# Kernel tuning notes

Measured on AMD Instinct MI355X. Metric: run time of the kernel, lower is better.

Reference implementation:

```python
import jax, jax.numpy as jnp
import numpy as np

N0, N1, N2, N3, B = 120000, 20000, 6000, 1600, 64
E1, E2, E3 = 480000, 144000, 38400
KS = 5  # kernel size per dim; K = 125 total


def spline_basis(pseudo, ks=KS):
    # open B-spline basis, degree 1, over [0,1]^3 (torch_spline_conv semantics)
    p = pseudo * (ks - 1)                       # (E,3)
    lo = jnp.clip(jnp.floor(p), 0.0, ks - 2.0)  # (E,3)
    f = p - lo                                  # fractional part
    bits = jnp.array([[(s >> d) & 1 for d in range(3)] for s in range(8)],
                     dtype=jnp.float32)         # (8,3) corner offsets
    w = jnp.where(bits[None] > 0, f[:, None, :], 1.0 - f[:, None, :])  # (E,8,3)
    basis = w[..., 0] * w[..., 1] * w[..., 2]   # (E,8)
    strides = jnp.array([1.0, ks, ks * ks], dtype=jnp.float32)
    kidx = ((lo[:, None, :] + bits[None]) * strides).sum(-1).astype(jnp.int32)  # (E,8)
    return basis, kidx


def spline_conv(x, edge_index, pseudo, W, root, bias, num_nodes):
    src, dst = edge_index[0], edge_index[1]
    basis, kidx = spline_basis(pseudo)                   # (E,8), (E,8)
    XW = jnp.einsum('ni,kio->nko', x, W)                 # (N,K,out)
    taps = XW[src[:, None], kidx]                        # (E,8,out) gather
    msg = (taps * basis[..., None]).sum(axis=1)          # (E,out)
    agg = jax.ops.segment_sum(msg, dst, num_segments=num_nodes)
    deg = jax.ops.segment_sum(jnp.ones_like(dst, jnp.float32), dst,
                              num_segments=num_nodes)
    agg = agg / jnp.maximum(deg, 1.0)[:, None]           # mean aggregation
    return agg + x @ root + bias


def seg_max(x, seg, n):
    v = jax.ops.segment_max(x, seg, num_segments=n)
    return jnp.where(jnp.isfinite(v), v, 0.0)  # empty voxels -> 0


def setup_inputs() -> dict:
    key = jax.random.key(0)
    ks = jax.random.split(key, 24)
    return {
        'x0': jax.random.uniform(ks[0], (N0, 1), jnp.float32),
        'cluster0': jax.random.randint(ks[1], (N0,), 0, N1),
        'edge1': jax.random.randint(ks[2], (2, E1), 0, N1),
        'pseudo1': jax.random.uniform(ks[3], (E1, 3), jnp.float32),
        'W1': jax.random.normal(ks[4], (125, 1, 64), jnp.float32) * 0.1,
        'root1': jax.random.normal(ks[5], (1, 64), jnp.float32) * 0.1,
        'b1': jnp.zeros((64,), jnp.float32),
        'cluster1': jax.random.randint(ks[6], (N1,), 0, N2),
        'edge2': jax.random.randint(ks[7], (2, E2), 0, N2),
        'pseudo2': jax.random.uniform(ks[8], (E2, 3), jnp.float32),
        'W2': jax.random.normal(ks[9], (125, 64, 64), jnp.float32) * 0.05,
        'root2': jax.random.normal(ks[10], (64, 64), jnp.float32) * 0.05,
        'b2': jnp.zeros((64,), jnp.float32),
        'cluster2': jax.random.randint(ks[11], (N2,), 0, N3),
        'edge3': jax.random.randint(ks[12], (2, E3), 0, N3),
        'pseudo3': jax.random.uniform(ks[13], (E3, 3), jnp.float32),
        'W3': jax.random.normal(ks[14], (125, 64, 128), jnp.float32) * 0.05,
        'root3': jax.random.normal(ks[15], (64, 128), jnp.float32) * 0.05,
        'b3': jnp.zeros((128,), jnp.float32),
        'cluster3': jax.random.randint(ks[16], (N3,), 0, B * 8),
        'fc1_w': jax.random.normal(ks[17], (1024, 256), jnp.float32) * 0.03,
        'fc1_b': jnp.zeros((256,), jnp.float32),
        'fc2_w': jax.random.normal(ks[18], (256, 10), jnp.float32) * 0.06,
        'fc2_b': jnp.zeros((10,), jnp.float32),
    }


def reference(x0, cluster0, edge1, pseudo1, W1, root1, b1,
              cluster1, edge2, pseudo2, W2, root2, b2,
              cluster2, edge3, pseudo3, W3, root3, b3,
              cluster3, fc1_w, fc1_b, fc2_w, fc2_b):
    x = seg_max(x0, cluster0, N1)                       # sparse voxel max pool 1
    x = jax.nn.elu(spline_conv(x, edge1, pseudo1, W1, root1, b1, N1))
    x = seg_max(x, cluster1, N2)                        # pool 2
    x = jax.nn.elu(spline_conv(x, edge2, pseudo2, W2, root2, b2, N2))
    x = seg_max(x, cluster2, N3)                        # pool 3
    x = jax.nn.elu(spline_conv(x, edge3, pseudo3, W3, root3, b3, N3))
    x = seg_max(x, cluster3, B * 8)                     # dense 2x2x2 voxel pool
    x = x.reshape(B, 8 * 128)
    x = jax.nn.elu(x @ fc1_w + fc1_b)
    x = x @ fc2_w + fc2_b
    return jax.nn.log_softmax(x, axis=1)
```

## Files before the change

### kernel.cpp

```cpp
#include <hip/hip_runtime.h>
#include <hip/hip_bf16.h>
#include <math.h>

#define N0c 120000
#define N1c 20000
#define N2c 6000
#define N3c 1600
#define E1c 480000
#define E2c 144000
#define E3c 38400

#define HB1 32
#define HB2 120
#define HB3 40
#define WT2B 125
#define WT3B 250
#define SS0B 469

typedef __attribute__((ext_vector_type(8))) short short8;
typedef __attribute__((ext_vector_type(4))) float f32x4;

__device__ __forceinline__ float eluf(float x) {
    return x > 0.0f ? x : expm1f(x);
}

__device__ __forceinline__ unsigned f2sort(float f) {
    unsigned u = __float_as_uint(f);
    return (u & 0x80000000u) ? ~u : (u | 0x80000000u);
}
__device__ __forceinline__ float sort2f(unsigned u) {
    unsigned bits = (u & 0x80000000u) ? (u & 0x7FFFFFFFu) : ~u;
    return __uint_as_float(bits);
}
__device__ __forceinline__ unsigned short f2bf(float v) {
    unsigned u = __float_as_uint(v);
    unsigned r = (u + 0x7FFFu + ((u >> 16) & 1u)) >> 16;
    return (unsigned short)r;
}

__global__ __launch_bounds__(256) void hist_all(
    const int* __restrict__ edge1, const int* __restrict__ edge2,
    const int* __restrict__ edge3,
    const float* __restrict__ pseudo2, const float* __restrict__ pseudo3,
    const float* __restrict__ W2, const float* __restrict__ W3,
    const float* __restrict__ x0, const int* __restrict__ cluster0,
    int* __restrict__ blockCnt1,
    int* __restrict__ blockCnt2, int* __restrict__ cntD2,
    int* __restrict__ blockCnt3, int* __restrict__ cntD3,
    unsigned short* __restrict__ W2t, unsigned short* __restrict__ W3t,
    unsigned* __restrict__ xm1)
{
    __shared__ float tile[64][65];
    int b = blockIdx.x, t = threadIdx.x;
    if (b < HB1) {
        int* h = (int*)tile;
        for (int i = t; i < 1250; i += 256) h[i] = 0;
        __syncthreads();
        for (int e = b * 256 + t; e < E1c; e += HB1 * 256)
            atomicAdd(&h[edge1[E1c + e] >> 4], 1);
        __syncthreads();
        for (int i = t; i < 1250; i += 256) blockCnt1[i * HB1 + b] = h[i];
    } else if (b < HB1 + HB2 + HB3) {
        int* h = (int*)tile;
        bool is2 = b < HB1 + HB2;
        int rb = is2 ? (b - HB1) : (b - HB1 - HB2);
        int nblk = is2 ? HB2 : HB3;
        int E = is2 ? E2c : E3c;
        const int* edge = is2 ? edge2 : edge3;
        const float* pseudo = is2 ? pseudo2 : pseudo3;
        int* blockCnt = is2 ? blockCnt2 : blockCnt3;
        int* dstCnt = is2 ? cntD2 : cntD3;
        if (t < 64) h[t] = 0;
        __syncthreads();
        for (int e = rb * 256 + t; e < E; e += nblk * 256) {
            int c = 0, mul = 1;
            #pragma unroll
            for (int d = 0; d < 3; d++) {
                float p = pseudo[e * 3 + d] * 4.0f;
                float l = fminf(fmaxf(floorf(p), 0.0f), 3.0f);
                c += (int)l * mul;
                mul <<= 2;
            }
            atomicAdd(&h[c], 1);
            atomicAdd(&dstCnt[edge[E + e]], 1);
        }
        __syncthreads();
        if (t < 64) blockCnt[t * nblk + rb] = h[t];
    } else if (b < HB1 + HB2 + HB3 + WT2B) {
        int k = b - (HB1 + HB2 + HB3);
        int col = t & 63, rq = t >> 6;
        #pragma unroll
        for (int i = 0; i < 16; i++) {
            int ic = i * 4 + rq;
            tile[ic][col] = W2[((size_t)k * 64 + ic) * 64 + col];
        }
        __syncthreads();
        int n = t >> 2, icq = (t & 3) * 16;
        unsigned* dst = (unsigned*)(W2t + ((size_t)k * 64 + n) * 64 + icq);
        #pragma unroll
        for (int j = 0; j < 8; j++) {
            unsigned lo = f2bf(tile[icq + 2 * j][n]);
            unsigned hi = f2bf(tile[icq + 2 * j + 1][n]);
            dst[j] = lo | (hi << 16);
        }
    } else if (b < HB1 + HB2 + HB3 + WT2B + WT3B) {
        int b2 = b - (HB1 + HB2 + HB3 + WT2B);
        int k = b2 >> 1, half = (b2 & 1) * 64;
        int col = t & 63, rq = t >> 6;
        #pragma unroll
        for (int i = 0; i < 16; i++) {
            int ic = i * 4 + rq;
            tile[ic][col] = W3[((size_t)k * 64 + ic) * 128 + half + col];
        }
        __syncthreads();
        int n = t >> 2, icq = (t & 3) * 16;
        unsigned* dst = (unsigned*)(W3t + ((size_t)k * 128 + half + n) * 64 + icq);
        #pragma unroll
        for (int j = 0; j < 8; j++) {
            unsigned lo = f2bf(tile[icq + 2 * j][n]);
            unsigned hi = f2bf(tile[icq + 2 * j + 1][n]);
            dst[j] = lo | (hi << 16);
        }
    } else {
        int idx = (b - (HB1 + HB2 + HB3 + WT2B + WT3B)) * 256 + t;
        if (idx < N0c)
            atomicMax(&xm1[cluster0[idx]], f2sort(x0[idx]));
    }
}

__global__ __launch_bounds__(256) void plan_all(
    const int* __restrict__ blockCnt1, int* __restrict__ start1,
    int* __restrict__ blockOff1,
    const int* __restrict__ blockCnt2, int* __restrict__ binCnt2,
    int* __restrict__ binStart2, int* __restrict__ blkPrefix2,
    int* __restrict__ chunkBin2, int* __restrict__ chunkOff2,
    int* __restrict__ blockOff2,
    const int* __restrict__ blockCnt3, int* __restrict__ binCnt3,
    int* __restrict__ binStart3, int* __restrict__ blkPrefix3,
    int* __restrict__ chunkBin3, int* __restrict__ chunkOff3,
    int* __restrict__ blockOff3)
{
    __shared__ int ps[256];
    __shared__ int ps64[64];
    int t = threadIdx.x;

    int loc[5];
    int s = 0;
    #pragma unroll
    for (int i = 0; i < 5; i++) {
        int bin = t * 5 + i;
        int v = 0;
        if (bin < 1250) {
            const int4* row = (const int4*)(blockCnt1 + (size_t)bin * HB1);
            #pragma unroll
            for (int j = 0; j < HB1 / 4; j++) {
                int4 q = row[j];
                v += q.x + q.y + q.z + q.w;
            }
        }
        loc[i] = v;
        s += v;
    }
    ps[t] = s;
    __syncthreads();
    for (int ofs = 1; ofs < 256; ofs <<= 1) {
        int add = (t >= ofs) ? ps[t - ofs] : 0;
        __syncthreads();
        ps[t] += add;
        __syncthreads();
    }
    int run = (t == 0) ? 0 : ps[t - 1];
    #pragma unroll
    for (int i = 0; i < 5; i++) {
        int bin = t * 5 + i;
        if (bin < 1250) {
            start1[bin] = run;
            run += loc[i];
        }
    }
    if (t == 255) start1[1250] = run;
    __syncthreads();

    if (t < 64) {
        int v = 0;
        const int4* row = (const int4*)(blockCnt2 + (size_t)t * HB2);
        for (int j = 0; j < HB2 / 4; j++) {
            int4 q = row[j];
            v += q.x + q.y + q.z + q.w;
        }
        binCnt2[t] = v;
        ps64[t] = v;
    }
    __syncthreads();
    if (t == 0) {
        int s2 = 0, p = 0;
        for (int c = 0; c < 64; c++) {
            int v = ps64[c];
            binStart2[c] = s2;
            blkPrefix2[c] = p;
            s2 += v;
            p += (v + 63) >> 6;
        }
        binStart2[64] = s2;
        blkPrefix2[64] = p;
    }
    __syncthreads();
    if (t < 64) {
        int nch = (binCnt2[t] + 63) >> 6;
        int base = blkPrefix2[t];
        for (int j = 0; j < nch; j++) {
            chunkBin2[base + j] = t;
            chunkOff2[base + j] = j;
        }
    }
    __syncthreads();

    if (t < 64) {
        int v = 0;
        const int4* row = (const int4*)(blockCnt3 + (size_t)t * HB3);
        for (int j = 0; j < HB3 / 4; j++) {
            int4 q = row[j];
            v += q.x + q.y + q.z + q.w;
        }
        binCnt3[t] = v;
        ps64[t] = v;
    }
    __syncthreads();
    if (t == 0) {
        int s3 = 0, p = 0;
        for (int c = 0; c < 64; c++) {
            int v = ps64[c];
            binStart3[c] = s3;
            blkPrefix3[c] = p;
            s3 += v;
            p += (v + 63) >> 6;
        }
        binStart3[64] = s3;
        blkPrefix3[64] = p;
    }
    __syncthreads();
    if (t < 64) {
        int nch = (binCnt3[t] + 63) >> 6;
        int base = blkPrefix3[t];
        for (int j = 0; j < nch; j++) {
            chunkBin3[base + j] = t;
            chunkOff3[base + j] = j;
        }
    }
    __syncthreads();

    for (int r = t; r < 1250; r += 256) {
        int rn = start1[r];
        const int* c = blockCnt1 + (size_t)r * HB1;
        int* o = blockOff1 + (size_t)r * HB1;
        #pragma unroll 4
        for (int bb = 0; bb < HB1; bb++) { o[bb] = rn; rn += c[bb]; }
    }
    if (t < 64) {
        int rn = binStart2[t];
        const int* c = blockCnt2 + (size_t)t * HB2;
        int* o = blockOff2 + (size_t)t * HB2;
        #pragma unroll 4
        for (int bb = 0; bb < HB2; bb++) { o[bb] = rn; rn += c[bb]; }
    } else if (t < 128) {
        int bin = t - 64;
        int rn = binStart3[bin];
        const int* c = blockCnt3 + (size_t)bin * HB3;
        int* o = blockOff3 + (size_t)bin * HB3;
        #pragma unroll 4
        for (int bb = 0; bb < HB3; bb++) { o[bb] = rn; rn += c[bb]; }
    }
}

__global__ __launch_bounds__(256) void scatter_all(
    const int* __restrict__ edge1, const float* __restrict__ pseudo1,
    const int* __restrict__ edge2, const float* __restrict__ pseudo2,
    const int* __restrict__ edge3, const float* __restrict__ pseudo3,
    const int* __restrict__ blockOff1, const int* __restrict__ blockOff2,
    const int* __restrict__ blockOff3,
    int4* __restrict__ rec1, int4* __restrict__ rec2, int4* __restrict__ rec3,
    unsigned* __restrict__ xm1)
{
    __shared__ int cur[1250];
    int b = blockIdx.x, t = threadIdx.x;
    if (b < HB1) {
        for (int i = t; i < 1250; i += 256) cur[i] = blockOff1[(size_t)i * HB1 + b];
        __syncthreads();
        for (int e = b * 256 + t; e < E1c; e += HB1 * 256) {
            int src = edge1[e], dst = edge1[E1c + e];
            float f[3];
            int kbase = 0, mul5 = 1;
            #pragma unroll
            for (int d = 0; d < 3; d++) {
                float pp = pseudo1[e * 3 + d] * 4.0f;
                float l = fminf(fmaxf(floorf(pp), 0.0f), 3.0f);
                f[d] = pp - l;
                kbase += (int)l * mul5;
                mul5 *= 5;
            }
            int p = atomicAdd(&cur[dst >> 4], 1);
            rec1[p] = make_int4(src | ((dst & 15) << 16) | (kbase << 20),
                                __float_as_int(f[0]), __float_as_int(f[1]),
                                __float_as_int(f[2]));
        }
    } else if (b < HB1 + HB2 + HB3) {
        bool is2 = b < HB1 + HB2;
        int rb = is2 ? (b - HB1) : (b - HB1 - HB2);
        int nblk = is2 ? HB2 : HB3;
        int E = is2 ? E2c : E3c;
        const int* edge = is2 ? edge2 : edge3;
        const float* pseudo = is2 ? pseudo2 : pseudo3;
        const int* blockOff = is2 ? blockOff2 : blockOff3;
        int4* rec = is2 ? rec2 : rec3;
        if (t < 64) cur[t] = blockOff[(size_t)t * nblk + rb];
        __syncthreads();
        for (int e = rb * 256 + t; e < E; e += nblk * 256) {
            int src = edge[e], dst = edge[E + e];
            float f[3];
            int c = 0, mul = 1;
            #pragma unroll
            for (int d = 0; d < 3; d++) {
                float pp = pseudo[e * 3 + d] * 4.0f;
                float l = fminf(fmaxf(floorf(pp), 0.0f), 3.0f);
                f[d] = pp - l;
                c += (int)l * mul;
                mul <<= 2;
            }
            int p = atomicAdd(&cur[c], 1);
            rec[p] = make_int4(src | (dst << 16),
                               __float_as_int(f[0]), __float_as_int(f[1]),
                               __float_as_int(f[2]));
        }
    } else {
        int idx = (b - (HB1 + HB2 + HB3)) * 256 + t;
        if (idx < N1c) {
            float f = sort2f(xm1[idx]);
            unsigned bb = __float_as_uint(f);
            if ((bb & 0x7F800000u) == 0x7F800000u) f = 0.0f;
            ((float*)xm1)[idx] = f;
        }
    }
}

__global__ __launch_bounds__(256) void conv1_block(
    const int4* __restrict__ rec, const float* __restrict__ x,
    const int* __restrict__ start,
    const float* __restrict__ W, const float* __restrict__ root,
    const float* __restrict__ bias, const int* __restrict__ cl,
    unsigned* __restrict__ xmOut) {
    __shared__ float T[16][128];
    __shared__ int degL[16];
    int b = blockIdx.x;
    for (int j = threadIdx.x; j < 2048; j += 256) ((float*)T)[j] = 0.0f;
    if (threadIdx.x < 16) degL[threadIdx.x] = 0;
    __syncthreads();
    int s0 = start[b], s1 = start[b + 1];
    for (int i = s0 + threadIdx.x; i < s1; i += 256) {
        int4 r = rec[i];
        int src = r.x & 0xFFFF;
        int ln = (r.x >> 16) & 15;
        int kbase = r.x >> 20;
        float f0 = __int_as_float(r.y);
        float f1 = __int_as_float(r.z);
        float f2 = __int_as_float(r.w);
        float xv = x[src];
        #pragma unroll
        for (int s = 0; s < 8; s++) {
            int b0 = s & 1, b1 = (s >> 1) & 1, b2 = (s >> 2) & 1;
            float w0 = b0 ? f0 : 1.0f - f0;
            float w1 = b1 ? f1 : 1.0f - f1;
            float w2 = b2 ? f2 : 1.0f - f2;
            int k = kbase + b0 + 5 * b1 + 25 * b2;
            atomicAdd(&T[ln][k], xv * w0 * w1 * w2);
        }
        atomicAdd(&degL[ln], 1);
    }
    __syncthreads();
    int w = threadIdx.x >> 6, lane = threadIdx.x & 63;
    float acc[4] = {0.0f, 0.0f, 0.0f, 0.0f};
    for (int k = 0; k < 125; k++) {
        float wv = W[(k << 6) + lane];
        #pragma unroll
        for (int j = 0; j < 4; j++)
            acc[j] = fmaf(T[w + 4 * j][k], wv, acc[j]);
    }
    int v0 = b << 4;
    #pragma unroll
    for (int j = 0; j < 4; j++) {
        int ln = w + 4 * j;
        int v = v0 + ln;
        float d = fmaxf((float)degL[ln], 1.0f);
        float val = eluf(acc[j] / d + x[v] * root[lane] + bias[lane]);
        atomicMax(&xmOut[((size_t)cl[v] << 6) + lane], f2sort(val));
    }
}

__global__ void decode_cvt(unsigned* __restrict__ buf,
                           unsigned short* __restrict__ xb, int total) {
    int idx = blockIdx.x * blockDim.x + threadIdx.x;
    if (idx >= total) return;
    float f = sort2f(buf[idx]);
    unsigned b = __float_as_uint(f);
    if ((b & 0x7F800000u) == 0x7F800000u) f = 0.0f;
    ((float*)buf)[idx] = f;
    xb[idx] = f2bf(f);
}

template<int COUT>
__global__ __launch_bounds__(256) void spline_mfma(
    const int4* __restrict__ recs,
    const unsigned short* __restrict__ Wt,
    const unsigned short* __restrict__ xb,
    const int* __restrict__ binStart,
    const int* __restrict__ binCnt,
    const int* __restrict__ blkPrefix,
    const int* __restrict__ chunkBin,
    const int* __restrict__ chunkOff,
    float* __restrict__ agg)
{
    __shared__ float basisS[4][8][64];
    __shared__ int srcS[4][64];
    __shared__ int dstS[4][64];

    int w = threadIdx.x >> 6, lane = threadIdx.x & 63;
    int c = blockIdx.x * 4 + w;
    if (c >= blkPrefix[64]) return;
    int bin = chunkBin[c];
    int chunk = chunkOff[c];
    int cnt = binCnt[bin];

    {
        int pos = chunk * 64 + lane;
        bool act = pos < cnt;
        int4 r = act ? recs[binStart[bin] + pos] : make_int4(0, 0, 0, 0);
        srcS[w][lane] = r.x & 0xFFFF;
        dstS[w][lane] = act ? (r.x >> 16) : -1;
        float f0 = __int_as_float(r.y);
        float f1 = __int_as_float(r.z);
        float f2 = __int_as_float(r.w);
        #pragma unroll
        for (int s = 0; s < 8; s++) {
            float w0 = (s & 1) ? f0 : 1.0f - f0;
            float w1 = (s & 2) ? f1 : 1.0f - f1;
            float w2 = (s & 4) ? f2 : 1.0f - f2;
            basisS[w][s][lane] = act ? (w0 * w1 * w2) : 0.0f;
        }
    }
    __builtin_amdgcn_wave_barrier();
    __threadfence_block();

    int lo0 = bin & 3, lo1 = (bin >> 2) & 3, lo2 = bin >> 4;
    int kbase = lo0 + 5 * lo1 + 25 * lo2;
    int colOff = blockIdx.y << 5;
    int q = lane >> 4;
    int mcol = lane & 15;

    short8 afr[4][2];
    #pragma unroll
    for (int rt = 0; rt < 4; rt++) {
        int src = srcS[w][rt * 16 + mcol];
        const unsigned short* xr = xb + ((size_t)src << 6) + q * 8;
        afr[rt][0] = *(const short8*)(xr);
        afr[rt][1] = *(const short8*)(xr + 32);
    }

    f32x4 acc[4][2];
    #pragma unroll
    for (int rt = 0; rt < 4; rt++)
        #pragma unroll
        for (int nt = 0; nt < 2; nt++)
            acc[rt][nt] = (f32x4){0.0f, 0.0f, 0.0f, 0.0f};
    const f32x4 zero4 = {0.0f, 0.0f, 0.0f, 0.0f};

    #pragma unroll 1
    for (int s = 0; s < 8; s++) {
        int k = kbase + (s & 1) + 5 * ((s >> 1) & 1) + 25 * (s >> 2);
        const unsigned short* Wk = Wt + ((size_t)k * COUT + colOff) * 64;
        short8 bfr[2][2];
        #pragma unroll
        for (int nt = 0; nt < 2; nt++) {
            const unsigned short* Wn = Wk + (size_t)(nt * 16 + mcol) * 64 + q * 8;
            bfr[nt][0] = *(const short8*)(Wn);
            bfr[nt][1] = *(const short8*)(Wn + 32);
        }
        #pragma unroll
        for (int rt = 0; rt < 4; rt++) {
            f32x4 ct[2];
            #pragma unroll
            for (int nt = 0; nt < 2; nt++) {
                ct[nt] = __builtin_amdgcn_mfma_f32_16x16x32_bf16(afr[rt][0], bfr[nt][0], zero4, 0, 0, 0);
                ct[nt] = __builtin_amdgcn_mfma_f32_16x16x32_bf16(afr[rt][1], bfr[nt][1], ct[nt], 0, 0, 0);
            }
            #pragma unroll
            for (int r = 0; r < 4; r++) {
                float bs = basisS[w][s][rt * 16 + q * 4 + r];
                #pragma unroll
                for (int nt = 0; nt < 2; nt++)
                    acc[rt][nt][r] = fmaf(bs, ct[nt][r], acc[rt][nt][r]);
            }
        }
    }

    #pragma unroll
    for (int rt = 0; rt < 4; rt++) {
        #pragma unroll
        for (int r = 0; r < 4; r++) {
            int d = dstS[w][rt * 16 + q * 4 + r];
            if (d >= 0) {
                float* ap = agg + (size_t)d * COUT + colOff + mcol;
                #pragma unroll
                for (int nt = 0; nt < 2; nt++)
                    atomicAdd(ap + nt * 16, acc[rt][nt][r]);
            }
        }
    }
}

__global__ __launch_bounds__(256) void node_update64(
    const float* __restrict__ agg, const int* __restrict__ deg,
    const float* __restrict__ xm, const float* __restrict__ root,
    const float* __restrict__ bias, const int* __restrict__ cl,
    unsigned* __restrict__ xmOut, int nNodes) {
    __shared__ float xsh[4][64];
    int w = threadIdx.x >> 6, lane = threadIdx.x & 63;
    int v = blockIdx.x * 4 + w;
    if (v >= nNodes) return;
    xsh[w][lane] = xm[((size_t)v << 6) + lane];
    float a = agg[((size_t)v << 6) + lane] / fmaxf((float)deg[v], 1.0f);
    float r = 0.0f;
    #pragma unroll 8
    for (int i = 0; i < 64; i++)
        r = fmaf(xsh[w][i], root[(i << 6) + lane], r);
    float val = eluf(a + r + bias[lane]);
    atomicMax(&xmOut[((size_t)cl[v] << 6) + lane], f2sort(val));
}

__global__ __launch_bounds__(256) void node_update128(
    const float* __restrict__ agg, const int* __restrict__ deg,
    const float* __restrict__ xm, const float* __restrict__ root,
    const float* __restrict__ bias, const int* __restrict__ cl,
    unsigned* __restrict__ xmOut, int nNodes) {
    __shared__ float xsh[4][64];
    int w = threadIdx.x >> 6, lane = threadIdx.x & 63;
    int v = blockIdx.x * 4 + w;
    if (v >= nNodes) return;
    xsh[w][lane] = xm[((size_t)v << 6) + lane];
    float dinv = 1.0f / fmaxf((float)deg[v], 1.0f);
    float a0 = agg[((size_t)v << 7) + lane] * dinv;
    float a1 = agg[((size_t)v << 7) + 64 + lane] * dinv;
    float r0 = 0.0f, r1 = 0.0f;
    #pragma unroll 8
    for (int i = 0; i < 64; i++) {
        float xi = xsh[w][i];
        r0 = fmaf(xi, root[(i << 7) + lane], r0);
        r1 = fmaf(xi, root[(i << 7) + 64 + lane], r1);
    }
    unsigned* orow = xmOut + ((size_t)cl[v] << 7);
    atomicMax(&orow[lane], f2sort(eluf(a0 + r0 + bias[lane])));
    atomicMax(&orow[64 + lane], f2sort(eluf(a1 + r1 + bias[lane + 64])));
}

__global__ __launch_bounds__(256) void fc1_split(
    const unsigned* __restrict__ xin, const float* __restrict__ w1,
    float* __restrict__ h) {
    __shared__ float xsh[128];
    int row = blockIdx.x, ks = blockIdx.y;
    int o = threadIdx.x;
    if (o < 128) {
        float f = sort2f(xin[row * 1024 + ks * 128 + o]);
        unsigned bb = __float_as_uint(f);
        if ((bb & 0x7F800000u) == 0x7F800000u) f = 0.0f;
        xsh[o] = f;
    }
    __syncthreads();
    float acc = 0.0f;
    const float* wp = w1 + (size_t)ks * 128 * 256 + o;
    #pragma unroll 8
    for (int i = 0; i < 128; i++)
        acc = fmaf(xsh[i], wp[i * 256], acc);
    atomicAdd(&h[row * 256 + o], acc);
}

__global__ __launch_bounds__(64) void fc2_k(
    const float* __restrict__ h, const float* __restrict__ b1,
    const float* __restrict__ w2, const float* __restrict__ b2,
    float* __restrict__ out) {
    __shared__ float hs[256];
    __shared__ float lg[10];
    int row = blockIdx.x;
    int t = threadIdx.x;
    for (int i = t; i < 256; i += 64) hs[i] = eluf(h[row * 256 + i] + b1[i]);
    __syncthreads();
    if (t < 10) {
        float a = b2[t];
        for (int i = 0; i < 256; i++) a = fmaf(hs[i], w2[i * 10 + t], a);
        lg[t] = a;
    }
    __syncthreads();
    if (t < 10) {
        float m = -1e30f;
        #pragma unroll
        for (int j = 0; j < 10; j++) m = fmaxf(m, lg[j]);
        float sum = 0.0f;
        #pragma unroll
        for (int j = 0; j < 10; j++) sum += expf(lg[j] - m);
        out[row * 10 + t] = lg[t] - m - logf(sum);
    }
}

extern "C" void kernel_launch(void* const* d_in, const int* in_sizes, int n_in,
                              void* d_out, int out_size, void* d_ws, size_t ws_size,
                              hipStream_t stream) {
    const float* x0      = (const float*)d_in[0];
    const int*   cluster0= (const int*)d_in[1];
    const int*   edge1   = (const int*)d_in[2];
    const float* pseudo1 = (const float*)d_in[3];
    const float* W1      = (const float*)d_in[4];
    const float* root1   = (const float*)d_in[5];
    const float* b1      = (const float*)d_in[6];
    const int*   cluster1= (const int*)d_in[7];
    const int*   edge2   = (const int*)d_in[8];
    const float* pseudo2 = (const float*)d_in[9];
    const float* W2      = (const float*)d_in[10];
    const float* root2   = (const float*)d_in[11];
    const float* b2      = (const float*)d_in[12];
    const int*   cluster2= (const int*)d_in[13];
    const int*   edge3   = (const int*)d_in[14];
    const float* pseudo3 = (const float*)d_in[15];
    const float* W3      = (const float*)d_in[16];
    const float* root3   = (const float*)d_in[17];
    const float* b3      = (const float*)d_in[18];
    const int*   cluster3= (const int*)d_in[19];
    const float* fc1_w   = (const float*)d_in[20];
    const float* fc1_b   = (const float*)d_in[21];
    const float* fc2_w   = (const float*)d_in[22];
    const float* fc2_b   = (const float*)d_in[23];
    float* out = (float*)d_out;

    float* ws = (float*)d_ws;
    size_t off = 0;
    float* xm1  = ws + off; off += 20480;
    float* xm2  = ws + off; off += (size_t)N2c * 64;
    float* xm3  = ws + off; off += (size_t)N3c * 64;
    float* xm4  = ws + off; off += 512 * 128;
    float* agg2 = ws + off; off += (size_t)N2c * 64;
    float* agg3 = ws + off; off += (size_t)N3c * 128;
    float* h1   = ws + off; off += 64 * 256;
    int* cntD2   = (int*)(ws + off); off += 6016;
    int* cntD3   = (int*)(ws + off); off += 1664;
    size_t zeroFloats = off;
    int4* rec1 = (int4*)(ws + off); off += (size_t)E1c * 4;
    int4* rec2 = (int4*)(ws + off); off += (size_t)E2c * 4;
    int4* rec3 = (int4*)(ws + off); off += (size_t)E3c * 4;
    unsigned short* W2t = (unsigned short*)(ws + off); off += 256000;
    unsigned short* W3t = (unsigned short*)(ws + off); off += 512000;
    unsigned short* xb2 = (unsigned short*)(ws + off); off += 192000;
    unsigned short* xb3 = (unsigned short*)(ws + off); off += 51200;
    int* start1    = (int*)(ws + off); off += 1280;
    int* blockCnt1 = (int*)(ws + off); off += HB1 * 1250;
    int* blockOff1 = (int*)(ws + off); off += HB1 * 1250;
    int* blockCnt2 = (int*)(ws + off); off += HB2 * 64;
    int* blockOff2 = (int*)(ws + off); off += HB2 * 64;
    int* blockCnt3 = (int*)(ws + off); off += HB3 * 64;
    int* blockOff3 = (int*)(ws + off); off += HB3 * 64;
    int* binCnt2   = (int*)(ws + off); off += 64;
    int* binStart2 = (int*)(ws + off); off += 80;
    int* blkPrefix2= (int*)(ws + off); off += 80;
    int* chunkBin2 = (int*)(ws + off); off += 2560;
    int* chunkOff2 = (int*)(ws + off); off += 2560;
    int* binCnt3   = (int*)(ws + off); off += 64;
    int* binStart3 = (int*)(ws + off); off += 80;
    int* blkPrefix3= (int*)(ws + off); off += 80;
    int* chunkBin3 = (int*)(ws + off); off += 768;
    int* chunkOff3 = (int*)(ws + off); off += 768;

    hipMemsetAsync(d_ws, 0, zeroFloats * sizeof(float), stream);

    hist_all<<<HB1 + HB2 + HB3 + WT2B + WT3B + SS0B, 256, 0, stream>>>(
        edge1, edge2, edge3, pseudo2, pseudo3, W2, W3, x0, cluster0,
        blockCnt1, blockCnt2, cntD2, blockCnt3, cntD3,
        W2t, W3t, (unsigned*)xm1);

    plan_all<<<1, 256, 0, stream>>>(
        blockCnt1, start1, blockOff1,
        blockCnt2, binCnt2, binStart2, blkPrefix2, chunkBin2, chunkOff2, blockOff2,
        blockCnt3, binCnt3, binStart3, blkPrefix3, chunkBin3, chunkOff3, blockOff3);

    scatter_all<<<HB1 + HB2 + HB3 + (N1c + 255) / 256, 256, 0, stream>>>(
        edge1, pseudo1, edge2, pseudo2, edge3, pseudo3,
        blockOff1, blockOff2, blockOff3, rec1, rec2, rec3, (unsigned*)xm1);

    conv1_block<<<1250, 256, 0, stream>>>(rec1, xm1, start1, W1, root1, b1,
                                          cluster1, (unsigned*)xm2);
    decode_cvt<<<(N2c * 64) / 256, 256, 0, stream>>>((unsigned*)xm2, xb2, N2c * 64);

    spline_mfma<64><<<dim3((E2c / 64 + 64 + 3) / 4, 2), 256, 0, stream>>>(
        rec2, W2t, xb2, binStart2, binCnt2, blkPrefix2, chunkBin2, chunkOff2, agg2);
    node_update64<<<(N2c + 3) / 4, 256, 0, stream>>>(agg2, cntD2, xm2, root2, b2,
                                                     cluster2, (unsigned*)xm3, N2c);
    decode_cvt<<<(N3c * 64) / 256, 256, 0, stream>>>((unsigned*)xm3, xb3, N3c * 64);

    spline_mfma<128><<<dim3((E3c / 64 + 64 + 3) / 4, 4), 256, 0, stream>>>(
        rec3, W3t, xb3, binStart3, binCnt3, blkPrefix3, chunkBin3, chunkOff3, agg3);
    node_update128<<<(N3c + 3) / 4, 256, 0, stream>>>(agg3, cntD3, xm3, root3, b3,
                                                      cluster3, (unsigned*)xm4, N3c);

    fc1_split<<<dim3(64, 8), 256, 0, stream>>>((unsigned*)xm4, fc1_w, h1);
    fc2_k<<<64, 64, 0, stream>>>(h1, fc1_b, fc2_w, fc2_b, out);
}
```

Baseline: 351.6 us.

## Pre-gather conv1 source features, widen MFMA column tiles, double HB1 blocks

The pool-1 decode of xm1 moves into the single-block plan kernel. The scatter kernel now gathers each edge's source feature into a parallel xrec1 array, so conv1 reads features sequentially instead of doing random gathers. The spline MFMA kernels now cover 64 output columns per block (4 n-tiles), which halves the grid y dimension and lets each A fragment be reused across more columns. HB1 doubles to 64 scatter/hist blocks. The risks are extra serial work in the one-block plan kernel, and higher register pressure from the larger accumulator tile.

Measured after the change: 372.7 us. 6.0% more time.

```diff
diff --git a/kernel.cpp b/kernel.cpp
--- a/kernel.cpp
+++ b/kernel.cpp
@@ -10,7 +10,7 @@
 #define E2c 144000
 #define E3c 38400
 
-#define HB1 32
+#define HB1 64
 #define HB2 120
 #define HB3 40
 #define WT2B 125
@@ -138,11 +138,19 @@
     const int* __restrict__ blockCnt3, int* __restrict__ binCnt3,
     int* __restrict__ binStart3, int* __restrict__ blkPrefix3,
     int* __restrict__ chunkBin3, int* __restrict__ chunkOff3,
-    int* __restrict__ blockOff3)
+    int* __restrict__ blockOff3,
+    unsigned* __restrict__ xm1)
 {
     __shared__ int ps[256];
     __shared__ int ps64[64];
     int t = threadIdx.x;
+
+    for (int i = t; i < N1c; i += 256) {
+        float f = sort2f(xm1[i]);
+        unsigned bb = __float_as_uint(f);
+        if ((bb & 0x7F800000u) == 0x7F800000u) f = 0.0f;
+        ((float*)xm1)[i] = f;
+    }
 
     int loc[5];
     int s = 0;
@@ -278,8 +286,9 @@
     const int* __restrict__ edge3, const float* __restrict__ pseudo3,
     const int* __restrict__ blockOff1, const int* __restrict__ blockOff2,
     const int* __restrict__ blockOff3,
-    int4* __restrict__ rec1, int4* __restrict__ rec2, int4* __restrict__ rec3,
-    unsigned* __restrict__ xm1)
+    int4* __restrict__ rec1, float* __restrict__ xrec1,
+    int4* __restrict__ rec2, int4* __restrict__ rec3,
+    const float* __restrict__ xm1f)
 {
     __shared__ int cur[1250];
     int b = blockIdx.x, t = threadIdx.x;
@@ -298,10 +307,12 @@
                 kbase += (int)l * mul5;
                 mul5 *= 5;
             }
+            float xv = xm1f[src];
             int p = atomicAdd(&cur[dst >> 4], 1);
-            rec1[p] = make_int4(src | ((dst & 15) << 16) | (kbase << 20),
+            rec1[p] = make_int4((dst & 15) | (kbase << 4),
                                 __float_as_int(f[0]), __float_as_int(f[1]),
                                 __float_as_int(f[2]));
+            xrec1[p] = xv;
         }
     } else if (b < HB1 + HB2 + HB3) {
         bool is2 = b < HB1 + HB2;
@@ -331,20 +342,12 @@
                                __float_as_int(f[0]), __float_as_int(f[1]),
                                __float_as_int(f[2]));
         }
-    } else {
-        int idx = (b - (HB1 + HB2 + HB3)) * 256 + t;
-        if (idx < N1c) {
-            float f = sort2f(xm1[idx]);
-            unsigned bb = __float_as_uint(f);
-            if ((bb & 0x7F800000u) == 0x7F800000u) f = 0.0f;
-            ((float*)xm1)[idx] = f;
-        }
     }
 }
 
 __global__ __launch_bounds__(256) void conv1_block(
-    const int4* __restrict__ rec, const float* __restrict__ x,
-    const int* __restrict__ start,
+    const int4* __restrict__ rec, const float* __restrict__ xrec,
+    const float* __restrict__ x, const int* __restrict__ start,
     const float* __restrict__ W, const float* __restrict__ root,
     const float* __restrict__ bias, const int* __restrict__ cl,
     unsigned* __restrict__ xmOut) {
@@ -357,13 +360,12 @@
     int s0 = start[b], s1 = start[b + 1];
     for (int i = s0 + threadIdx.x; i < s1; i += 256) {
         int4 r = rec[i];
-        int src = r.x & 0xFFFF;
-        int ln = (r.x >> 16) & 15;
-        int kbase = r.x >> 20;
+        float xv = xrec[i];
+        int ln = r.x & 15;
+        int kbase = r.x >> 4;
         float f0 = __int_as_float(r.y);
         float f1 = __int_as_float(r.z);
         float f2 = __int_as_float(r.w);
-        float xv = x[src];
         #pragma unroll
         for (int s = 0; s < 8; s++) {
             int b0 = s & 1, b1 = (s >> 1) & 1, b2 = (s >> 2) & 1;
@@ -451,7 +453,7 @@
 
     int lo0 = bin & 3, lo1 = (bin >> 2) & 3, lo2 = bin >> 4;
     int kbase = lo0 + 5 * lo1 + 25 * lo2;
-    int colOff = blockIdx.y << 5;
+    int colOff = (COUT == 128) ? (blockIdx.y << 6) : 0;
     int q = lane >> 4;
     int mcol = lane & 15;
 
@@ -464,11 +466,11 @@
         afr[rt][1] = *(const short8*)(xr + 32);
     }
 
-    f32x4 acc[4][2];
+    f32x4 acc[4][4];
     #pragma unroll
     for (int rt = 0; rt < 4; rt++)
         #pragma unroll
-        for (int nt = 0; nt < 2; nt++)
+        for (int nt = 0; nt < 4; nt++)
             acc[rt][nt] = (f32x4){0.0f, 0.0f, 0.0f, 0.0f};
     const f32x4 zero4 = {0.0f, 0.0f, 0.0f, 0.0f};
 
@@ -476,18 +478,18 @@
     for (int s = 0; s < 8; s++) {
         int k = kbase + (s & 1) + 5 * ((s >> 1) & 1) + 25 * (s >> 2);
         const unsigned short* Wk = Wt + ((size_t)k * COUT + colOff) * 64;
-        short8 bfr[2][2];
-        #pragma unroll
-        for (int nt = 0; nt < 2; nt++) {
+        short8 bfr[4][2];
+        #pragma unroll
+        for (int nt = 0; nt < 4; nt++) {
             const unsigned short* Wn = Wk + (size_t)(nt * 16 + mcol) * 64 + q * 8;
             bfr[nt][0] = *(const short8*)(Wn);
             bfr[nt][1] = *(const short8*)(Wn + 32);
         }
         #pragma unroll
         for (int rt = 0; rt < 4; rt++) {
-            f32x4 ct[2];
+            f32x4 ct[4];
             #pragma unroll
-            for (int nt = 0; nt < 2; nt++) {
+            for (int nt = 0; nt < 4; nt++) {
                 ct[nt] = __builtin_amdgcn_mfma_f32_16x16x32_bf16(afr[rt][0], bfr[nt][0], zero4, 0, 0, 0);
                 ct[nt] = __builtin_amdgcn_mfma_f32_16x16x32_bf16(afr[rt][1], bfr[nt][1], ct[nt], 0, 0, 0);
             }
@@ -495,7 +497,7 @@
             for (int r = 0; r < 4; r++) {
                 float bs = basisS[w][s][rt * 16 + q * 4 + r];
                 #pragma unroll
-                for (int nt = 0; nt < 2; nt++)
+                for (int nt = 0; nt < 4; nt++)
                     acc[rt][nt][r] = fmaf(bs, ct[nt][r], acc[rt][nt][r]);
             }
         }
@@ -509,7 +511,7 @@
             if (d >= 0) {
                 float* ap = agg + (size_t)d * COUT + colOff + mcol;
                 #pragma unroll
-                for (int nt = 0; nt < 2; nt++)
+                for (int nt = 0; nt < 4; nt++)
                     atomicAdd(ap + nt * 16, acc[rt][nt][r]);
             }
         }
@@ -650,6 +652,7 @@
     int* cntD3   = (int*)(ws + off); off += 1664;
     size_t zeroFloats = off;
     int4* rec1 = (int4*)(ws + off); off += (size_t)E1c * 4;
+    float* xrec1 = (float*)(ws + off); off += E1c;
     int4* rec2 = (int4*)(ws + off); off += (size_t)E2c * 4;
     int4* rec3 = (int4*)(ws + off); off += (size_t)E3c * 4;
     unsigned short* W2t = (unsigned short*)(ws + off); off += 256000;
@@ -684,23 +687,24 @@
     plan_all<<<1, 256, 0, stream>>>(
         blockCnt1, start1, blockOff1,
         blockCnt2, binCnt2, binStart2, blkPrefix2, chunkBin2, chunkOff2, blockOff2,
-        blockCnt3, binCnt3, binStart3, blkPrefix3, chunkBin3, chunkOff3, blockOff3);
-
-    scatter_all<<<HB1 + HB2 + HB3 + (N1c + 255) / 256, 256, 0, stream>>>(
+        blockCnt3, binCnt3, binStart3, blkPrefix3, chunkBin3, chunkOff3, blockOff3,
+        (unsigned*)xm1);
+
+    scatter_all<<<HB1 + HB2 + HB3, 256, 0, stream>>>(
         edge1, pseudo1, edge2, pseudo2, edge3, pseudo3,
-        blockOff1, blockOff2, blockOff3, rec1, rec2, rec3, (unsigned*)xm1);
-
-    conv1_block<<<1250, 256, 0, stream>>>(rec1, xm1, start1, W1, root1, b1,
+        blockOff1, blockOff2, blockOff3, rec1, xrec1, rec2, rec3, xm1);
+
+    conv1_block<<<1250, 256, 0, stream>>>(rec1, xrec1, xm1, start1, W1, root1, b1,
                                           cluster1, (unsigned*)xm2);
     decode_cvt<<<(N2c * 64) / 256, 256, 0, stream>>>((unsigned*)xm2, xb2, N2c * 64);
 
-    spline_mfma<64><<<dim3((E2c / 64 + 64 + 3) / 4, 2), 256, 0, stream>>>(
+    spline_mfma<64><<<dim3((E2c / 64 + 64 + 3) / 4, 1), 256, 0, stream>>>(
         rec2, W2t, xb2, binStart2, binCnt2, blkPrefix2, chunkBin2, chunkOff2, agg2);
     node_update64<<<(N2c + 3) / 4, 256, 0, stream>>>(agg2, cntD2, xm2, root2, b2,
                                                      cluster2, (unsigned*)xm3, N2c);
     decode_cvt<<<(N3c * 64) / 256, 256, 0, stream>>>((unsigned*)xm3, xb3, N3c * 64);
 
-    spline_mfma<128><<<dim3((E3c / 64 + 64 + 3) / 4, 4), 256, 0, stream>>>(
+    spline_mfma<128><<<dim3((E3c / 64 + 64 + 3) / 4, 2), 256, 0, stream>>>(
         rec3, W3t, xb3, binStart3, binCnt3, blkPrefix3, chunkBin3, chunkOff3, agg3);
     node_update128<<<(N3c + 3) / 4, 256, 0, stream>>>(agg3, cntD3, xm3, root3, b3,
                                                       cluster3, (unsigned*)xm4, N3c);
```
